# Performance work log

Hardware: AMD Instinct MI355X
Metric: run time of the kernel (lower is better)

Reference implementation:

```python
import jax, jax.numpy as jnp
import numpy as np


def P1(X):
    # Projection onto {X : X @ 1 = 1, 1^T X = 1} under Frobenius norm.
    # Expanding the original matrix expression:
    #   P1(X)[i,j] = X[i,j] + 1/n + sum(X)/n^2 - row_sum[i]/n - col_sum[j]/n
    n = X.shape[1]
    row = X.sum(axis=1, keepdims=True)          # [n,1]
    col = X.sum(axis=0, keepdims=True)          # [1,n]
    s = row.sum()                               # scalar total
    return X + (1.0 / n + s / (n * n)) - row / n - col / n


def setup_inputs() -> dict:
    key = jax.random.key(0)
    n = 4096
    X = jax.random.normal(key, (n, n), dtype=jnp.float32)
    return {"X": X, "max_iters": 20}


def reference(X, max_iters):
    # Dykstra-style alternating projection: X <- P1(X); early-return if
    # min(X) >= 0, else X <- relu(X); up to max_iters iterations.
    # Fixed-length scan with a `done` flag reproduces the data-dependent
    # early exit while staying jit-compatible.
    def step(carry, _):
        Xc, done = carry
        Xp = P1(Xc)
        nonneg = jnp.min(Xp) >= 0
        # If converged this iter: return the un-relu'd projection; else relu.
        Xn = jnp.where(nonneg, Xp, jax.nn.relu(Xp))
        Xout = jnp.where(done, Xc, Xn)
        return (Xout, done | nonneg), None

    (Xf, _), _ = jax.lax.scan(step, (X, jnp.array(False)), None, length=max_iters)
    return Xf
```

## Files before the change

### kernel.cpp

```cpp
#include <hip/hip_runtime.h>


#define NN    4096
#define NV4   1024
#define NBLK  256
#define ITERS 20
#define INV_N (1.0f / 4096.0f)

typedef unsigned long long u64;
typedef float f32x4 __attribute__((ext_vector_type(4)));

__device__ __forceinline__ float wave_reduce_sum(float v) {
    #pragma unroll
    for (int m = 1; m < 64; m <<= 1) v += __shfl_xor(v, m, 64);
    return v;
}
__device__ __forceinline__ void st_b64(u64* p, u64 v) {
    __hip_atomic_store(p, v, __ATOMIC_RELAXED, __HIP_MEMORY_SCOPE_AGENT);
}
__device__ __forceinline__ u64 ld_b64(const u64* p) {
    return __hip_atomic_load(p, __ATOMIC_RELAXED, __HIP_MEMORY_SCOPE_AGENT);
}
__device__ __forceinline__ u64 packf2(float a, float b) {
    return (u64)__float_as_uint(a) | ((u64)__float_as_uint(b) << 32);
}
__device__ __forceinline__ float lo32(u64 u) { return __uint_as_float((unsigned)u); }
__device__ __forceinline__ float hi32(u64 u) { return __uint_as_float((unsigned)(u >> 32)); }

__global__ __launch_bounds__(1024, 4)
void persist12(const float* __restrict__ X0, float* __restrict__ Xout,
               u64* __restrict__ colF,
               u64* __restrict__ rowF,
               u64* __restrict__ pflag)
{
    const int t    = threadIdx.x;
    const int lane = t & 63;
    const int g    = t >> 6;
    const int c    = lane;
    const int b    = blockIdx.x;
    const int bi   = b >> 4;
    const int bj   = b & 15;

    __shared__ float part[16][64][17];
    __shared__ f32x4 cqA[16][64];
    __shared__ f32x4 cqB[16][64];
    __shared__ f32x4 rqB[16][64];
    __shared__ float bsv[256];

    f32x4 x[16];
    {
        const f32x4* xi = (const f32x4*)X0;
        const size_t base = (size_t)(bi * 256 + g * 16) * NV4 + (bj * 64 + c);
        #pragma unroll
        for (int r = 0; r < 16; ++r)
            x[r] = xi[base + (size_t)r * NV4];
    }

    for (int iter = 0; iter < ITERS; ++iter) {
        const int p = iter & 1;
        const u64 tagv = (u64)(iter + 1);

        f32x4 cacc = x[0];
        #pragma unroll
        for (int r = 1; r < 16; ++r) cacc += x[r];
        cqA[g][c] = cacc;
        #pragma unroll
        for (int r = 0; r < 16; ++r)
            part[g][c][r] = (x[r].x + x[r].y) + (x[r].z + x[r].w);
        __syncthreads();

        float bs = 0.f;
        if (g == 0) {
            f32x4 vq = cqA[0][c];
            #pragma unroll
            for (int k = 1; k < 16; ++k) vq += cqA[k][c];
            u64* dst = colF + (((size_t)(p * NBLK + b)) << 7) + 2 * c;
            st_b64(dst,     packf2(vq.x, vq.y));
            st_b64(dst + 1, packf2(vq.z, vq.w));
            bs = wave_reduce_sum((vq.x + vq.y) + (vq.z + vq.w));
        }
        {
            const int r_ = lane & 15, q_ = lane >> 4;
            float v = 0.f;
            #pragma unroll
            for (int k = 0; k < 16; ++k) v += part[g][q_ * 16 + k][r_];
            v += __shfl_xor(v, 16, 64);
            v += __shfl_xor(v, 32, 64);
            float vp = __shfl_xor(v, 1, 64);
            if (lane < 16 && (lane & 1) == 0)
                st_b64(rowF + (((size_t)(p * NBLK + b)) << 7) + 8 * g + (lane >> 1),
                       packf2(v, vp));
        }
        asm volatile("s_waitcnt vmcnt(0)" ::: "memory");
        __syncthreads();
        if (t == 0)
            st_b64(pflag + ((size_t)(p * NBLK + b) << 3),
                   (tagv << 32) | (u64)__float_as_uint(bs));

        const int fcsrc = g * 16 + bj;
        const int frsrc = bi * 16 + g;
        {
            const u64* fc = pflag + ((size_t)(p * NBLK + fcsrc) << 3);
            const u64* fr = pflag + ((size_t)(p * NBLK + frsrc) << 3);
            const u64* fb = pflag + ((size_t)(p * NBLK + (t & 255)) << 3);
            bool dc = false, dr = false, db = (t >= 256);
            u64 ub = 0;
            while (!(dc && dr)) {
                if (!dc && (ld_b64(fc) >> 32) == tagv) dc = true;
                if (!dr && (ld_b64(fr) >> 32) == tagv) dr = true;
                if (!db) { u64 u = ld_b64(fb);
                           if ((u >> 32) == tagv) { ub = u; db = true; } }
                if (!(dc && dr)) __builtin_amdgcn_s_sleep(1);
            }
            asm volatile("" ::: "memory");
            {
                const u64* cp = colF + (((size_t)(p * NBLK + fcsrc)) << 7) + 2 * c;
                const u64* rp = rowF + (((size_t)(p * NBLK + frsrc)) << 7) + 2 * c;
                u64 c0 = ld_b64(cp), c1 = ld_b64(cp + 1);
                u64 r0 = ld_b64(rp), r1 = ld_b64(rp + 1);
                f32x4 cv, rv;
                cv.x = lo32(c0); cv.y = hi32(c0); cv.z = lo32(c1); cv.w = hi32(c1);
                rv.x = lo32(r0); rv.y = hi32(r0); rv.z = lo32(r1); rv.w = hi32(r1);
                cqB[g][c] = cv;
                rqB[g][c] = rv;
            }
            while (!db) {
                u64 u = ld_b64(fb);
                if ((u >> 32) == tagv) { ub = u; db = true; }
                else __builtin_amdgcn_s_sleep(1);
            }
            if (t < 256) bsv[t] = lo32(ub);
        }
        asm volatile("" ::: "memory");
        __syncthreads();

        float vb = bsv[lane] + bsv[64 + lane] + bsv[128 + lane] + bsv[192 + lane];
        const float sG = wave_reduce_sum(vb);
        f32x4 cs = cqB[0][c];
        #pragma unroll
        for (int k = 1; k < 16; ++k) cs += cqB[k][c];
        float vr;
        {
            const int rr = lane & 15, kk = lane >> 4;
            const float* rqf = (const float*)&rqB[0][0];
            vr = 0.f;
            #pragma unroll
            for (int j = 0; j < 4; ++j)
                vr += rqf[(((4 * kk + j) * 64) + (4 * g + (rr >> 2))) * 4 + (rr & 3)];
            vr += __shfl_xor(vr, 16, 64);
            vr += __shfl_xor(vr, 32, 64);
        }

        const float cc0 = INV_N + sG * (INV_N * INV_N);
        const f32x4 csub = cs * INV_N;
        #pragma unroll
        for (int r = 0; r < 16; ++r) {
            const float rwr = __shfl(vr, r, 64);
            const float a = cc0 - rwr * INV_N;
            x[r].x = fmaxf(x[r].x + a - csub.x, 0.f);
            x[r].y = fmaxf(x[r].y + a - csub.y, 0.f);
            x[r].z = fmaxf(x[r].z + a - csub.z, 0.f);
            x[r].w = fmaxf(x[r].w + a - csub.w, 0.f);
        }
    }

    {
        f32x4* xo = (f32x4*)Xout;
        const size_t base = (size_t)(bi * 256 + g * 16) * NV4 + (bj * 64 + c);
        #pragma unroll
        for (int r = 0; r < 16; ++r)
            xo[base + (size_t)r * NV4] = x[r];
    }
}

extern "C" void kernel_launch(void* const* d_in, const int* in_sizes, int n_in,
                              void* d_out, int out_size, void* d_ws, size_t ws_size,
                              hipStream_t stream)
{
    const float* X0 = (const float*)d_in[0];
    float* X = (float*)d_out;

    u64* colF  = (u64*)d_ws;
    u64* rowF  = colF + 2 * NBLK * 128;
    u64* pflag = rowF + 2 * NBLK * 128;

    hipMemsetAsync((void*)pflag, 0, 2 * NBLK * 8 * sizeof(u64), stream);

    persist12<<<dim3(NBLK), dim3(1024), 0, stream>>>(X0, X, colF, rowF, pflag);
}
```

Before: 242.4 us.

## Replace per-block flag barrier with per-value tagged partial sums

Each column, row and block-sum partial is now stored as a 64-bit word carrying the iteration tag next to the float. Consumers poll the data words directly instead of waiting on a separate per-block flag. This removes the vmcnt drain, the extra __syncthreads before publishing and the flag round-trip, so each wave can start consuming as soon as its own data arrives. In exchange the bytes written and polled per iteration double, the memset grows to cover all tagged buffers, and the row reduction is now done with shuffles across the polled quads.

After: 314.7 us. 29.8% more time.

```diff
diff --git a/kernel.cpp b/kernel.cpp
--- a/kernel.cpp
+++ b/kernel.cpp
@@ -21,17 +21,27 @@
 __device__ __forceinline__ u64 ld_b64(const u64* p) {
     return __hip_atomic_load(p, __ATOMIC_RELAXED, __HIP_MEMORY_SCOPE_AGENT);
 }
-__device__ __forceinline__ u64 packf2(float a, float b) {
-    return (u64)__float_as_uint(a) | ((u64)__float_as_uint(b) << 32);
+__device__ __forceinline__ u64 tagf(u64 tagv, float x) {
+    return (tagv << 32) | (u64)__float_as_uint(x);
 }
 __device__ __forceinline__ float lo32(u64 u) { return __uint_as_float((unsigned)u); }
-__device__ __forceinline__ float hi32(u64 u) { return __uint_as_float((unsigned)(u >> 32)); }
+
+__device__ __forceinline__ f32x4 poll_quad(const u64* p, u64 tagv) {
+    u64 a = ld_b64(p), b = ld_b64(p + 1), c = ld_b64(p + 2), d = ld_b64(p + 3);
+    while (((a >> 32) != tagv) | ((b >> 32) != tagv) |
+           ((c >> 32) != tagv) | ((d >> 32) != tagv)) {
+        __builtin_amdgcn_s_sleep(1);
+        a = ld_b64(p); b = ld_b64(p + 1); c = ld_b64(p + 2); d = ld_b64(p + 3);
+    }
+    f32x4 r; r.x = lo32(a); r.y = lo32(b); r.z = lo32(c); r.w = lo32(d);
+    return r;
+}
 
 __global__ __launch_bounds__(1024, 4)
-void persist12(const float* __restrict__ X0, float* __restrict__ Xout,
+void persist13(const float* __restrict__ X0, float* __restrict__ Xout,
                u64* __restrict__ colF,
                u64* __restrict__ rowF,
-               u64* __restrict__ pflag)
+               u64* __restrict__ gsB)
 {
     const int t    = threadIdx.x;
     const int lane = t & 63;
@@ -44,7 +54,7 @@
     __shared__ float part[16][64][17];
     __shared__ f32x4 cqA[16][64];
     __shared__ f32x4 cqB[16][64];
-    __shared__ f32x4 rqB[16][64];
+    __shared__ float sbsL[16];
     __shared__ float bsv[256];
 
     f32x4 x[16];
@@ -67,95 +77,87 @@
         #pragma unroll
         for (int r = 0; r < 16; ++r)
             part[g][c][r] = (x[r].x + x[r].y) + (x[r].z + x[r].w);
+        asm volatile("s_waitcnt lgkmcnt(0)" ::: "memory");
+        float v;
+        {
+            const int r_ = lane & 15, q_ = lane >> 4;
+            v = 0.f;
+            #pragma unroll
+            for (int k = 0; k < 16; ++k) v += part[g][q_ * 16 + k][r_];
+            v += __shfl_xor(v, 16, 64);
+            v += __shfl_xor(v, 32, 64);
+        }
+        if (lane < 16)
+            st_b64(rowF + (((size_t)(p * NBLK + b)) << 8) + 16 * g + lane,
+                   tagf(tagv, v));
+        {
+            float v2 = v;
+            v2 += __shfl_xor(v2, 1, 64); v2 += __shfl_xor(v2, 2, 64);
+            v2 += __shfl_xor(v2, 4, 64); v2 += __shfl_xor(v2, 8, 64);
+            if (lane == 0) sbsL[g] = v2;
+        }
         __syncthreads();
 
-        float bs = 0.f;
         if (g == 0) {
             f32x4 vq = cqA[0][c];
             #pragma unroll
             for (int k = 1; k < 16; ++k) vq += cqA[k][c];
-            u64* dst = colF + (((size_t)(p * NBLK + b)) << 7) + 2 * c;
-            st_b64(dst,     packf2(vq.x, vq.y));
-            st_b64(dst + 1, packf2(vq.z, vq.w));
-            bs = wave_reduce_sum((vq.x + vq.y) + (vq.z + vq.w));
+            u64* dst = colF + (((size_t)(p * NBLK + b)) << 8) + 4 * c;
+            st_b64(dst,     tagf(tagv, vq.x));
+            st_b64(dst + 1, tagf(tagv, vq.y));
+            st_b64(dst + 2, tagf(tagv, vq.z));
+            st_b64(dst + 3, tagf(tagv, vq.w));
+        } else if (g == 1) {
+            float sv = sbsL[lane & 15];
+            sv += __shfl_xor(sv, 1, 64); sv += __shfl_xor(sv, 2, 64);
+            sv += __shfl_xor(sv, 4, 64); sv += __shfl_xor(sv, 8, 64);
+            if (lane == 0)
+                st_b64(gsB + ((size_t)(p * NBLK + b) << 3), tagf(tagv, sv));
+        }
+
+        f32x4 rq;
+        {
+            const int j = lane >> 2, rqi = lane & 3;
+            const u64* rp = rowF + (((size_t)(p * NBLK + bi * 16 + j)) << 8)
+                                 + 16 * g + 4 * rqi;
+            f32x4 rv = poll_quad(rp, tagv);
+            #pragma unroll
+            for (int m = 4; m <= 32; m <<= 1) {
+                rv.x += __shfl_xor(rv.x, m, 64);
+                rv.y += __shfl_xor(rv.y, m, 64);
+                rv.z += __shfl_xor(rv.z, m, 64);
+                rv.w += __shfl_xor(rv.w, m, 64);
+            }
+            rq = rv;
         }
         {
-            const int r_ = lane & 15, q_ = lane >> 4;
-            float v = 0.f;
-            #pragma unroll
-            for (int k = 0; k < 16; ++k) v += part[g][q_ * 16 + k][r_];
-            v += __shfl_xor(v, 16, 64);
-            v += __shfl_xor(v, 32, 64);
-            float vp = __shfl_xor(v, 1, 64);
-            if (lane < 16 && (lane & 1) == 0)
-                st_b64(rowF + (((size_t)(p * NBLK + b)) << 7) + 8 * g + (lane >> 1),
-                       packf2(v, vp));
+            const u64* cp = colF + (((size_t)(p * NBLK + g * 16 + bj)) << 8) + 4 * c;
+            cqB[g][c] = poll_quad(cp, tagv);
         }
-        asm volatile("s_waitcnt vmcnt(0)" ::: "memory");
-        __syncthreads();
-        if (t == 0)
-            st_b64(pflag + ((size_t)(p * NBLK + b) << 3),
-                   (tagv << 32) | (u64)__float_as_uint(bs));
-
-        const int fcsrc = g * 16 + bj;
-        const int frsrc = bi * 16 + g;
-        {
-            const u64* fc = pflag + ((size_t)(p * NBLK + fcsrc) << 3);
-            const u64* fr = pflag + ((size_t)(p * NBLK + frsrc) << 3);
-            const u64* fb = pflag + ((size_t)(p * NBLK + (t & 255)) << 3);
-            bool dc = false, dr = false, db = (t >= 256);
-            u64 ub = 0;
-            while (!(dc && dr)) {
-                if (!dc && (ld_b64(fc) >> 32) == tagv) dc = true;
-                if (!dr && (ld_b64(fr) >> 32) == tagv) dr = true;
-                if (!db) { u64 u = ld_b64(fb);
-                           if ((u >> 32) == tagv) { ub = u; db = true; } }
-                if (!(dc && dr)) __builtin_amdgcn_s_sleep(1);
+        if (t < 256) {
+            const u64* gp = gsB + ((size_t)(p * NBLK + t) << 3);
+            u64 u = ld_b64(gp);
+            while ((u >> 32) != tagv) {
+                __builtin_amdgcn_s_sleep(1);
+                u = ld_b64(gp);
             }
-            asm volatile("" ::: "memory");
-            {
-                const u64* cp = colF + (((size_t)(p * NBLK + fcsrc)) << 7) + 2 * c;
-                const u64* rp = rowF + (((size_t)(p * NBLK + frsrc)) << 7) + 2 * c;
-                u64 c0 = ld_b64(cp), c1 = ld_b64(cp + 1);
-                u64 r0 = ld_b64(rp), r1 = ld_b64(rp + 1);
-                f32x4 cv, rv;
-                cv.x = lo32(c0); cv.y = hi32(c0); cv.z = lo32(c1); cv.w = hi32(c1);
-                rv.x = lo32(r0); rv.y = hi32(r0); rv.z = lo32(r1); rv.w = hi32(r1);
-                cqB[g][c] = cv;
-                rqB[g][c] = rv;
-            }
-            while (!db) {
-                u64 u = ld_b64(fb);
-                if ((u >> 32) == tagv) { ub = u; db = true; }
-                else __builtin_amdgcn_s_sleep(1);
-            }
-            if (t < 256) bsv[t] = lo32(ub);
+            bsv[t] = lo32(u);
         }
         asm volatile("" ::: "memory");
         __syncthreads();
 
-        float vb = bsv[lane] + bsv[64 + lane] + bsv[128 + lane] + bsv[192 + lane];
-        const float sG = wave_reduce_sum(vb);
         f32x4 cs = cqB[0][c];
         #pragma unroll
         for (int k = 1; k < 16; ++k) cs += cqB[k][c];
-        float vr;
-        {
-            const int rr = lane & 15, kk = lane >> 4;
-            const float* rqf = (const float*)&rqB[0][0];
-            vr = 0.f;
-            #pragma unroll
-            for (int j = 0; j < 4; ++j)
-                vr += rqf[(((4 * kk + j) * 64) + (4 * g + (rr >> 2))) * 4 + (rr & 3)];
-            vr += __shfl_xor(vr, 16, 64);
-            vr += __shfl_xor(vr, 32, 64);
-        }
+        float vb = bsv[lane] + bsv[64 + lane] + bsv[128 + lane] + bsv[192 + lane];
+        const float sG = wave_reduce_sum(vb);
 
         const float cc0 = INV_N + sG * (INV_N * INV_N);
         const f32x4 csub = cs * INV_N;
+        const float rqa[4] = {rq.x, rq.y, rq.z, rq.w};
         #pragma unroll
         for (int r = 0; r < 16; ++r) {
-            const float rwr = __shfl(vr, r, 64);
+            const float rwr = __shfl(rqa[r & 3], r >> 2, 64);
             const float a = cc0 - rwr * INV_N;
             x[r].x = fmaxf(x[r].x + a - csub.x, 0.f);
             x[r].y = fmaxf(x[r].y + a - csub.y, 0.f);
@@ -180,11 +182,13 @@
     const float* X0 = (const float*)d_in[0];
     float* X = (float*)d_out;
 
-    u64* colF  = (u64*)d_ws;
-    u64* rowF  = colF + 2 * NBLK * 128;
-    u64* pflag = rowF + 2 * NBLK * 128;
+    u64* colF = (u64*)d_ws;
+    u64* rowF = colF + 2 * NBLK * 256;
+    u64* gsB  = rowF + 2 * NBLK * 256;
 
-    hipMemsetAsync((void*)pflag, 0, 2 * NBLK * 8 * sizeof(u64), stream);
+    const size_t tagged_bytes =
+        (size_t)(2 * NBLK * 256 + 2 * NBLK * 256 + 2 * NBLK * 8) * sizeof(u64);
+    hipMemsetAsync((void*)colF, 0, tagged_bytes, stream);
 
-    persist12<<<dim3(NBLK), dim3(1024), 0, stream>>>(X0, X, colF, rowF, pflag);
+    persist13<<<dim3(NBLK), dim3(1024), 0, stream>>>(X0, X, colF, rowF, gsB);
 }
```

## Tag each published row/column partial sum with its iteration to drop flag ordering

Applied to the files above, without the earlier changes.

Each row and column partial sum is now stored as its own 64-bit word carrying the iteration tag. Consumers poll the data words directly until the tags match, instead of trusting a per-block flag. This removes the s_waitcnt vmcnt(0) and one block-wide barrier before the flag is published, and lets row sums go out before the column reduction. The cost is twice the workspace footprint and cross-block traffic, plus a larger memset of tagged buffers before launch.

Result: slower. 279.1 us (+15.1%).

```diff
diff --git a/kernel.cpp b/kernel.cpp
--- a/kernel.cpp
+++ b/kernel.cpp
@@ -21,17 +21,27 @@
 __device__ __forceinline__ u64 ld_b64(const u64* p) {
     return __hip_atomic_load(p, __ATOMIC_RELAXED, __HIP_MEMORY_SCOPE_AGENT);
 }
-__device__ __forceinline__ u64 packf2(float a, float b) {
-    return (u64)__float_as_uint(a) | ((u64)__float_as_uint(b) << 32);
+__device__ __forceinline__ u64 tagf(u64 tagv, float x) {
+    return (tagv << 32) | (u64)__float_as_uint(x);
 }
 __device__ __forceinline__ float lo32(u64 u) { return __uint_as_float((unsigned)u); }
-__device__ __forceinline__ float hi32(u64 u) { return __uint_as_float((unsigned)(u >> 32)); }
+
+__device__ __forceinline__ f32x4 gather_quad(const u64* p, u64 tagv) {
+    u64 a = ld_b64(p), b = ld_b64(p + 1), c = ld_b64(p + 2), d = ld_b64(p + 3);
+    while (((a >> 32) != tagv) | ((b >> 32) != tagv) |
+           ((c >> 32) != tagv) | ((d >> 32) != tagv)) {
+        __builtin_amdgcn_s_sleep(1);
+        a = ld_b64(p); b = ld_b64(p + 1); c = ld_b64(p + 2); d = ld_b64(p + 3);
+    }
+    f32x4 r; r.x = lo32(a); r.y = lo32(b); r.z = lo32(c); r.w = lo32(d);
+    return r;
+}
 
 __global__ __launch_bounds__(1024, 4)
-void persist12(const float* __restrict__ X0, float* __restrict__ Xout,
+void persist14(const float* __restrict__ X0, float* __restrict__ Xout,
                u64* __restrict__ colF,
                u64* __restrict__ rowF,
-               u64* __restrict__ pflag)
+               u64* __restrict__ gsB)
 {
     const int t    = threadIdx.x;
     const int lane = t & 63;
@@ -67,18 +77,7 @@
         #pragma unroll
         for (int r = 0; r < 16; ++r)
             part[g][c][r] = (x[r].x + x[r].y) + (x[r].z + x[r].w);
-        __syncthreads();
-
-        float bs = 0.f;
-        if (g == 0) {
-            f32x4 vq = cqA[0][c];
-            #pragma unroll
-            for (int k = 1; k < 16; ++k) vq += cqA[k][c];
-            u64* dst = colF + (((size_t)(p * NBLK + b)) << 7) + 2 * c;
-            st_b64(dst,     packf2(vq.x, vq.y));
-            st_b64(dst + 1, packf2(vq.z, vq.w));
-            bs = wave_reduce_sum((vq.x + vq.y) + (vq.z + vq.w));
-        }
+        asm volatile("s_waitcnt lgkmcnt(0)" ::: "memory");
         {
             const int r_ = lane & 15, q_ = lane >> 4;
             float v = 0.f;
@@ -86,23 +85,33 @@
             for (int k = 0; k < 16; ++k) v += part[g][q_ * 16 + k][r_];
             v += __shfl_xor(v, 16, 64);
             v += __shfl_xor(v, 32, 64);
-            float vp = __shfl_xor(v, 1, 64);
-            if (lane < 16 && (lane & 1) == 0)
-                st_b64(rowF + (((size_t)(p * NBLK + b)) << 7) + 8 * g + (lane >> 1),
-                       packf2(v, vp));
+            if (lane < 16)
+                st_b64(rowF + (((size_t)(p * NBLK + b)) << 8) + 16 * g + lane,
+                       tagf(tagv, v));
         }
-        asm volatile("s_waitcnt vmcnt(0)" ::: "memory");
         __syncthreads();
-        if (t == 0)
-            st_b64(pflag + ((size_t)(p * NBLK + b) << 3),
-                   (tagv << 32) | (u64)__float_as_uint(bs));
+
+        if (g == 0) {
+            f32x4 vq = cqA[0][c];
+            #pragma unroll
+            for (int k = 1; k < 16; ++k) vq += cqA[k][c];
+            u64* dst = colF + (((size_t)(p * NBLK + b)) << 8) + 4 * c;
+            st_b64(dst,     tagf(tagv, vq.x));
+            st_b64(dst + 1, tagf(tagv, vq.y));
+            st_b64(dst + 2, tagf(tagv, vq.z));
+            st_b64(dst + 3, tagf(tagv, vq.w));
+            float bs = wave_reduce_sum((vq.x + vq.y) + (vq.z + vq.w));
+            asm volatile("" ::: "memory");
+            if (lane == 0)
+                st_b64(gsB + ((size_t)(p * NBLK + b) << 3), tagf(tagv, bs));
+        }
 
         const int fcsrc = g * 16 + bj;
         const int frsrc = bi * 16 + g;
         {
-            const u64* fc = pflag + ((size_t)(p * NBLK + fcsrc) << 3);
-            const u64* fr = pflag + ((size_t)(p * NBLK + frsrc) << 3);
-            const u64* fb = pflag + ((size_t)(p * NBLK + (t & 255)) << 3);
+            const u64* fc = gsB + ((size_t)(p * NBLK + fcsrc) << 3);
+            const u64* fr = gsB + ((size_t)(p * NBLK + frsrc) << 3);
+            const u64* fb = gsB + ((size_t)(p * NBLK + (t & 255)) << 3);
             bool dc = false, dr = false, db = (t >= 256);
             u64 ub = 0;
             while (!(dc && dr)) {
@@ -114,15 +123,10 @@
             }
             asm volatile("" ::: "memory");
             {
-                const u64* cp = colF + (((size_t)(p * NBLK + fcsrc)) << 7) + 2 * c;
-                const u64* rp = rowF + (((size_t)(p * NBLK + frsrc)) << 7) + 2 * c;
-                u64 c0 = ld_b64(cp), c1 = ld_b64(cp + 1);
-                u64 r0 = ld_b64(rp), r1 = ld_b64(rp + 1);
-                f32x4 cv, rv;
-                cv.x = lo32(c0); cv.y = hi32(c0); cv.z = lo32(c1); cv.w = hi32(c1);
-                rv.x = lo32(r0); rv.y = hi32(r0); rv.z = lo32(r1); rv.w = hi32(r1);
-                cqB[g][c] = cv;
-                rqB[g][c] = rv;
+                const u64* cp = colF + (((size_t)(p * NBLK + fcsrc)) << 8) + 4 * c;
+                const u64* rp = rowF + (((size_t)(p * NBLK + frsrc)) << 8) + 4 * c;
+                cqB[g][c] = gather_quad(cp, tagv);
+                rqB[g][c] = gather_quad(rp, tagv);
             }
             while (!db) {
                 u64 u = ld_b64(fb);
@@ -180,11 +184,13 @@
     const float* X0 = (const float*)d_in[0];
     float* X = (float*)d_out;
 
-    u64* colF  = (u64*)d_ws;
-    u64* rowF  = colF + 2 * NBLK * 128;
-    u64* pflag = rowF + 2 * NBLK * 128;
+    u64* colF = (u64*)d_ws;
+    u64* rowF = colF + 2 * NBLK * 256;
+    u64* gsB  = rowF + 2 * NBLK * 256;
 
-    hipMemsetAsync((void*)pflag, 0, 2 * NBLK * 8 * sizeof(u64), stream);
+    const size_t tagged_bytes =
+        (size_t)(2 * NBLK * 256 + 2 * NBLK * 256 + 2 * NBLK * 8) * sizeof(u64);
+    hipMemsetAsync((void*)colF, 0, tagged_bytes, stream);
 
-    persist12<<<dim3(NBLK), dim3(1024), 0, stream>>>(X0, X, colF, rowF, pflag);
+    persist14<<<dim3(NBLK), dim3(1024), 0, stream>>>(X0, X, colF, rowF, gsB);
 }
```

## Split exchange polling: waves 0-7 gather column partials, waves 8-15 gather row partials

Applied to the files above, without the earlier changes.

The cross-block exchange is reassigned so the first eight waves each poll two column-peer flags and pre-add their column partials, and the last eight waves each poll two row-peer flags and pre-add their row partials. Before, every wave polled one column peer and one row peer. The shared-memory reduction after the barrier now sums 8 entries instead of 16, and the row-sum shuffle reduction is replaced by a direct indexed read. The change aims to cut per-wave global loads and the LDS reduction work in the synchronisation-bound inner loop. In exchange, each wave now waits on two peers of the same type, which may lengthen the critical wait for some waves.

Measured after the change: 239.7 us. No clear change (-1.1%).

```diff
diff --git a/kernel.cpp b/kernel.cpp
--- a/kernel.cpp
+++ b/kernel.cpp
@@ -28,7 +28,7 @@
 __device__ __forceinline__ float hi32(u64 u) { return __uint_as_float((unsigned)(u >> 32)); }
 
 __global__ __launch_bounds__(1024, 4)
-void persist12(const float* __restrict__ X0, float* __restrict__ Xout,
+void persist17(const float* __restrict__ X0, float* __restrict__ Xout,
                u64* __restrict__ colF,
                u64* __restrict__ rowF,
                u64* __restrict__ pflag)
@@ -43,8 +43,8 @@
 
     __shared__ float part[16][64][17];
     __shared__ f32x4 cqA[16][64];
-    __shared__ f32x4 cqB[16][64];
-    __shared__ f32x4 rqB[16][64];
+    __shared__ f32x4 cqB[8][64];
+    __shared__ f32x4 rqB[8][64];
     __shared__ float bsv[256];
 
     f32x4 x[16];
@@ -97,32 +97,30 @@
             st_b64(pflag + ((size_t)(p * NBLK + b) << 3),
                    (tagv << 32) | (u64)__float_as_uint(bs));
 
-        const int fcsrc = g * 16 + bj;
-        const int frsrc = bi * 16 + g;
-        {
-            const u64* fc = pflag + ((size_t)(p * NBLK + fcsrc) << 3);
-            const u64* fr = pflag + ((size_t)(p * NBLK + frsrc) << 3);
+        if (g < 8) {
+            const int p0 = 32 * g + bj, p1 = 32 * g + 16 + bj;
+            const u64* f0 = pflag + ((size_t)(p * NBLK + p0) << 3);
+            const u64* f1 = pflag + ((size_t)(p * NBLK + p1) << 3);
             const u64* fb = pflag + ((size_t)(p * NBLK + (t & 255)) << 3);
-            bool dc = false, dr = false, db = (t >= 256);
+            bool d0 = false, d1 = false, db = (t >= 256);
             u64 ub = 0;
-            while (!(dc && dr)) {
-                if (!dc && (ld_b64(fc) >> 32) == tagv) dc = true;
-                if (!dr && (ld_b64(fr) >> 32) == tagv) dr = true;
+            while (!(d0 && d1)) {
+                if (!d0 && (ld_b64(f0) >> 32) == tagv) d0 = true;
+                if (!d1 && (ld_b64(f1) >> 32) == tagv) d1 = true;
                 if (!db) { u64 u = ld_b64(fb);
                            if ((u >> 32) == tagv) { ub = u; db = true; } }
-                if (!(dc && dr)) __builtin_amdgcn_s_sleep(1);
+                if (!(d0 && d1)) __builtin_amdgcn_s_sleep(1);
             }
             asm volatile("" ::: "memory");
             {
-                const u64* cp = colF + (((size_t)(p * NBLK + fcsrc)) << 7) + 2 * c;
-                const u64* rp = rowF + (((size_t)(p * NBLK + frsrc)) << 7) + 2 * c;
-                u64 c0 = ld_b64(cp), c1 = ld_b64(cp + 1);
-                u64 r0 = ld_b64(rp), r1 = ld_b64(rp + 1);
-                f32x4 cv, rv;
-                cv.x = lo32(c0); cv.y = hi32(c0); cv.z = lo32(c1); cv.w = hi32(c1);
-                rv.x = lo32(r0); rv.y = hi32(r0); rv.z = lo32(r1); rv.w = hi32(r1);
+                const u64* c0p = colF + (((size_t)(p * NBLK + p0)) << 7) + 2 * c;
+                const u64* c1p = colF + (((size_t)(p * NBLK + p1)) << 7) + 2 * c;
+                u64 a0 = ld_b64(c0p), a1 = ld_b64(c0p + 1);
+                u64 b0 = ld_b64(c1p), b1 = ld_b64(c1p + 1);
+                f32x4 cv;
+                cv.x = lo32(a0) + lo32(b0); cv.y = hi32(a0) + hi32(b0);
+                cv.z = lo32(a1) + lo32(b1); cv.w = hi32(a1) + hi32(b1);
                 cqB[g][c] = cv;
-                rqB[g][c] = rv;
             }
             while (!db) {
                 u64 u = ld_b64(fb);
@@ -130,6 +128,26 @@
                 else __builtin_amdgcn_s_sleep(1);
             }
             if (t < 256) bsv[t] = lo32(ub);
+        } else {
+            const int w = g - 8;
+            const int q0 = bi * 16 + 2 * w, q1 = q0 + 1;
+            const u64* f0 = pflag + ((size_t)(p * NBLK + q0) << 3);
+            const u64* f1 = pflag + ((size_t)(p * NBLK + q1) << 3);
+            bool d0 = false, d1 = false;
+            while (!(d0 && d1)) {
+                if (!d0 && (ld_b64(f0) >> 32) == tagv) d0 = true;
+                if (!d1 && (ld_b64(f1) >> 32) == tagv) d1 = true;
+                if (!(d0 && d1)) __builtin_amdgcn_s_sleep(1);
+            }
+            asm volatile("" ::: "memory");
+            const u64* r0p = rowF + (((size_t)(p * NBLK + q0)) << 7) + 2 * c;
+            const u64* r1p = rowF + (((size_t)(p * NBLK + q1)) << 7) + 2 * c;
+            u64 a0 = ld_b64(r0p), a1 = ld_b64(r0p + 1);
+            u64 b0 = ld_b64(r1p), b1 = ld_b64(r1p + 1);
+            f32x4 rv;
+            rv.x = lo32(a0) + lo32(b0); rv.y = hi32(a0) + hi32(b0);
+            rv.z = lo32(a1) + lo32(b1); rv.w = hi32(a1) + hi32(b1);
+            rqB[w][c] = rv;
         }
         asm volatile("" ::: "memory");
         __syncthreads();
@@ -138,24 +156,17 @@
         const float sG = wave_reduce_sum(vb);
         f32x4 cs = cqB[0][c];
         #pragma unroll
-        for (int k = 1; k < 16; ++k) cs += cqB[k][c];
-        float vr;
-        {
-            const int rr = lane & 15, kk = lane >> 4;
-            const float* rqf = (const float*)&rqB[0][0];
-            vr = 0.f;
-            #pragma unroll
-            for (int j = 0; j < 4; ++j)
-                vr += rqf[(((4 * kk + j) * 64) + (4 * g + (rr >> 2))) * 4 + (rr & 3)];
-            vr += __shfl_xor(vr, 16, 64);
-            vr += __shfl_xor(vr, 32, 64);
-        }
+        for (int k = 1; k < 8; ++k) cs += cqB[k][c];
+        f32x4 rq4 = rqB[0][4 * g + (lane & 3)];
+        #pragma unroll
+        for (int k = 1; k < 8; ++k) rq4 += rqB[k][4 * g + (lane & 3)];
+        const float rqa[4] = {rq4.x, rq4.y, rq4.z, rq4.w};
 
         const float cc0 = INV_N + sG * (INV_N * INV_N);
         const f32x4 csub = cs * INV_N;
         #pragma unroll
         for (int r = 0; r < 16; ++r) {
-            const float rwr = __shfl(vr, r, 64);
+            const float rwr = __shfl(rqa[r & 3], r >> 2, 64);
             const float a = cc0 - rwr * INV_N;
             x[r].x = fmaxf(x[r].x + a - csub.x, 0.f);
             x[r].y = fmaxf(x[r].y + a - csub.y, 0.f);
@@ -186,5 +197,5 @@
 
     hipMemsetAsync((void*)pflag, 0, 2 * NBLK * 8 * sizeof(u64), stream);
 
-    persist12<<<dim3(NBLK), dim3(1024), 0, stream>>>(X0, X, colF, rowF, pflag);
-}
+    persist17<<<dim3(NBLK), dim3(1024), 0, stream>>>(X0, X, colF, rowF, pflag);
+}
```
